# Kernel tuning notes

Hardware: AMD Instinct MI355X
Metric: run time of the kernel (lower is better)

The kernel has to match this reference:

```python
import jax, jax.numpy as jnp
import numpy as np

N, E = 100000, 1600000
IN_DIM, OUT_DIM, EDGE_DIM = 128, 64, 32
H, HD = 4, 16  # num_heads, head_dim; H*HD == OUT_DIM
NEG_SLOPE = 0.2


def setup_inputs() -> dict:
    key = jax.random.key(0)
    ks = jax.random.split(key, 9)
    return {
        "node_feat": jax.random.normal(ks[0], (N, IN_DIM), jnp.float32),
        "edge_feat": jax.random.normal(ks[1], (E, EDGE_DIM), jnp.float32),
        "W_src": jax.random.normal(ks[2], (OUT_DIM, IN_DIM), jnp.float32) * (2.0 / np.sqrt(IN_DIM + OUT_DIM)),
        "W_dst": jax.random.normal(ks[3], (OUT_DIM, IN_DIM), jnp.float32) * (2.0 / np.sqrt(IN_DIM + OUT_DIM)),
        "W_edge": jax.random.normal(ks[4], (OUT_DIM, EDGE_DIM), jnp.float32) * (2.0 / np.sqrt(EDGE_DIM + OUT_DIM)),
        "attn": jax.random.normal(ks[5], (1, H, HD), jnp.float32) * (2.0 / np.sqrt(1 + HD)),
        "bias": jnp.zeros((OUT_DIM,), jnp.float32),
        "src": jax.random.randint(ks[6], (E,), 0, N, jnp.int32),
        "dst": jax.random.randint(ks[7], (E,), 0, N, jnp.int32),
    }


def reference(node_feat, edge_feat, W_src, W_dst, W_edge, attn, bias, src, dst):
    n = node_feat.shape[0]
    # Linear projections (dropout is identity in eval mode / p=0)
    feat_src = (node_feat @ W_src.T).reshape(n, H, HD)  # [N,H,HD]
    feat_dst = (node_feat @ W_dst.T).reshape(n, H, HD)  # [N,H,HD]
    e_edge = (edge_feat @ W_edge.T).reshape(-1, H, HD)  # [E,H,HD]

    # u_add_v gather + edge feature injection, GATv2 nonlinearity then attn dot
    e = feat_src[src] + feat_dst[dst] + e_edge          # [E,H,HD]
    e = jax.nn.leaky_relu(e, NEG_SLOPE)
    logits = jnp.sum(e * attn, axis=-1)                 # [E,H]

    # edge softmax: normalize over edges sharing the same destination node
    seg_max = jax.ops.segment_max(logits, dst, num_segments=n)      # [N,H]
    ex = jnp.exp(logits - seg_max[dst])                             # [E,H]
    seg_sum = jax.ops.segment_sum(ex, dst, num_segments=n)          # [N,H]
    alpha = ex / seg_sum[dst]                                       # [E,H]

    # u_mul_e message + sum-aggregate to destinations
    msg = feat_src[src] * alpha[:, :, None]                         # [E,H,HD]
    ft = jax.ops.segment_sum(msg.reshape(-1, H * HD), dst, num_segments=n)  # [N,OUT]
    rst = ft + bias
    return rst, alpha
```

## Files before the change

kernel.cpp:

```cpp
#include <hip/hip_runtime.h>
#include <hip/hip_bf16.h>

#define N_NODES 100000
#define N_EDGES 1600000
#define IN_DIM 128
#define OUT_DIM 64
#define EDGE_DIM 32
#define NH 4
#define HD 16
#define NEG_SLOPE 0.2f

#define W_SRC_ELEMS (OUT_DIM * IN_DIM)
#define W_EDGE_ELEMS (OUT_DIM * EDGE_DIM)
#define W_TOTAL (2 * W_SRC_ELEMS + W_EDGE_ELEMS)

typedef __attribute__((ext_vector_type(8))) short short8;
typedef __attribute__((ext_vector_type(4))) float floatx4;

__device__ __forceinline__ void cvt_hilo(const float* __restrict__ p, short8& hi, short8& lo)
{
    floatx4 x0 = *(const floatx4*)p;
    floatx4 x1 = *(const floatx4*)(p + 4);
    float v[8] = {x0[0], x0[1], x0[2], x0[3], x1[0], x1[1], x1[2], x1[3]};
#pragma unroll
    for (int j = 0; j < 8; ++j) {
        union { __hip_bfloat16 b; short s; } h, l;
        h.b = __float2bfloat16(v[j]);
        l.b = __float2bfloat16(v[j] - __bfloat162float(h.b));
        hi[j] = h.s;
        lo[j] = l.s;
    }
}

__device__ __forceinline__ void cvt_hilo_nt(const float* __restrict__ p, short8& hi, short8& lo)
{
    floatx4 x0 = __builtin_nontemporal_load((const floatx4*)p);
    floatx4 x1 = __builtin_nontemporal_load((const floatx4*)(p + 4));
    float v[8] = {x0[0], x0[1], x0[2], x0[3], x1[0], x1[1], x1[2], x1[3]};
#pragma unroll
    for (int j = 0; j < 8; ++j) {
        union { __hip_bfloat16 b; short s; } h, l;
        h.b = __float2bfloat16(v[j]);
        l.b = __float2bfloat16(v[j] - __bfloat162float(h.b));
        hi[j] = h.s;
        lo[j] = l.s;
    }
}

__global__ __launch_bounds__(256) void wsplit_kernel(
    const float* __restrict__ W_src,
    const float* __restrict__ W_dst,
    const float* __restrict__ W_edge,
    short* __restrict__ w_hi,
    short* __restrict__ w_lo)
{
    int g = blockIdx.x * 256 + threadIdx.x;
    if (g >= W_TOTAL) return;
    float v;
    if (g < W_SRC_ELEMS)            v = W_src[g];
    else if (g < 2 * W_SRC_ELEMS)   v = W_dst[g - W_SRC_ELEMS];
    else                            v = W_edge[g - 2 * W_SRC_ELEMS];
    union { __hip_bfloat16 b; short s; } h, l;
    h.b = __float2bfloat16(v);
    l.b = __float2bfloat16(v - __bfloat162float(h.b));
    w_hi[g] = h.s;
    w_lo[g] = l.s;
}

__global__ __launch_bounds__(64) void node_proj_kernel(
    const float* __restrict__ node_feat,
    const short* __restrict__ w_hi,
    const short* __restrict__ w_lo,
    float* __restrict__ feat_src,
    float* __restrict__ feat_dst)
{
    const int lane = threadIdx.x;
    const int col  = lane & 15;
    const int quad = lane >> 4;
    const int m0   = blockIdx.x * 16;

    floatx4 acc[8];
#pragma unroll
    for (int t = 0; t < 8; ++t) acc[t] = (floatx4){0.f, 0.f, 0.f, 0.f};

#pragma unroll
    for (int kc = 0; kc < 4; ++kc) {
        short8 ahi, alo;
        cvt_hilo_nt(node_feat + (size_t)(m0 + col) * IN_DIM + kc * 32 + quad * 8, ahi, alo);
#pragma unroll
        for (int t = 0; t < 8; ++t) {
            int o = (t < 4 ? 0 : OUT_DIM) + (t & 3) * 16 + col;
            size_t off = (size_t)o * IN_DIM + kc * 32 + quad * 8;
            short8 bhi = *(const short8*)(w_hi + off);
            short8 blo = *(const short8*)(w_lo + off);
            acc[t] = __builtin_amdgcn_mfma_f32_16x16x32_bf16(ahi, bhi, acc[t], 0, 0, 0);
            acc[t] = __builtin_amdgcn_mfma_f32_16x16x32_bf16(ahi, blo, acc[t], 0, 0, 0);
            acc[t] = __builtin_amdgcn_mfma_f32_16x16x32_bf16(alo, bhi, acc[t], 0, 0, 0);
        }
    }

#pragma unroll
    for (int t = 0; t < 8; ++t) {
        float* out = (t < 4) ? feat_src : feat_dst;
        int ob = (t & 3) * 16;
#pragma unroll
        for (int r = 0; r < 4; ++r) {
            int node = m0 + quad * 4 + r;
            out[(size_t)node * OUT_DIM + ob + col] = acc[t][r];
        }
    }
}

__global__ __launch_bounds__(256) void edge_logits_kernel(
    const float* __restrict__ edge_feat,
    const short* __restrict__ we_hi,
    const short* __restrict__ we_lo,
    const float* __restrict__ attn,
    const int* __restrict__ src,
    const int* __restrict__ dst,
    const float* __restrict__ feat_src,
    const float* __restrict__ feat_dst,
    float* __restrict__ ex_out,
    int* __restrict__ deg)
{
    const int lane = threadIdx.x & 63;
    const int wave = threadIdx.x >> 6;
    const int col  = lane & 15;
    const int quad = lane >> 4;
    const size_t ebase0 = ((size_t)blockIdx.x * 4 + wave) * 32;

    int s[2][4], d[2][4];
#pragma unroll
    for (int u = 0; u < 2; ++u)
#pragma unroll
        for (int r = 0; r < 4; ++r) {
            s[u][r] = __builtin_nontemporal_load(&src[ebase0 + u * 16 + quad * 4 + r]);
            d[u][r] = __builtin_nontemporal_load(&dst[ebase0 + u * 16 + quad * 4 + r]);
        }

    short8 ahi[2], alo[2];
#pragma unroll
    for (int u = 0; u < 2; ++u)
        cvt_hilo_nt(edge_feat + (ebase0 + u * 16 + col) * EDGE_DIM + quad * 8, ahi[u], alo[u]);

    float att[4];
#pragma unroll
    for (int t = 0; t < 4; ++t) att[t] = attn[t * 16 + col];

    floatx4 acc[2][4];
#pragma unroll
    for (int t = 0; t < 4; ++t) {
        size_t off = (size_t)(t * 16 + col) * EDGE_DIM + quad * 8;
        short8 bhi = *(const short8*)(we_hi + off);
        short8 blo = *(const short8*)(we_lo + off);
#pragma unroll
        for (int u = 0; u < 2; ++u) {
            floatx4 c = (floatx4){0.f, 0.f, 0.f, 0.f};
            c = __builtin_amdgcn_mfma_f32_16x16x32_bf16(ahi[u], bhi, c, 0, 0, 0);
            c = __builtin_amdgcn_mfma_f32_16x16x32_bf16(ahi[u], blo, c, 0, 0, 0);
            c = __builtin_amdgcn_mfma_f32_16x16x32_bf16(alo[u], bhi, c, 0, 0, 0);
            acc[u][t] = c;
        }
    }

    const int j = col;
    const int rsel = j >> 2;

#pragma unroll
    for (int u = 0; u < 2; ++u) {
        float p[16];
#pragma unroll
        for (int r = 0; r < 4; ++r)
#pragma unroll
            for (int t = 0; t < 4; ++t) {
                float v = acc[u][t][r]
                        + feat_src[(size_t)s[u][r] * OUT_DIM + t * 16 + col]
                        + feat_dst[(size_t)d[u][r] * OUT_DIM + t * 16 + col];
                v = (v > 0.f) ? v : NEG_SLOPE * v;
                p[r * 4 + t] = v * att[t];
            }

        {
            const bool u8 = (col & 8) != 0;
#pragma unroll
            for (int i = 0; i < 8; ++i) {
                float keep = u8 ? p[i + 8] : p[i];
                float send = u8 ? p[i] : p[i + 8];
                p[i] = keep + __shfl_xor(send, 8);
            }
            const bool u4 = (col & 4) != 0;
#pragma unroll
            for (int i = 0; i < 4; ++i) {
                float keep = u4 ? p[i + 4] : p[i];
                float send = u4 ? p[i] : p[i + 4];
                p[i] = keep + __shfl_xor(send, 4);
            }
            const bool u2 = (col & 2) != 0;
#pragma unroll
            for (int i = 0; i < 2; ++i) {
                float keep = u2 ? p[i + 2] : p[i];
                float send = u2 ? p[i] : p[i + 2];
                p[i] = keep + __shfl_xor(send, 2);
            }
            const bool u1 = (col & 1) != 0;
            {
                float keep = u1 ? p[1] : p[0];
                float send = u1 ? p[0] : p[1];
                p[0] = keep + __shfl_xor(send, 1);
            }
        }

        float ev = __expf(p[0]);
        __builtin_nontemporal_store(ev, &ex_out[(ebase0 + u * 16) * NH + lane]);

        int dd = d[u][0];
#pragma unroll
        for (int r = 1; r < 4; ++r) dd = (rsel == r) ? d[u][r] : dd;
        if ((j & 3) == 0) atomicAdd(&deg[dd], 1);
    }
}

#define SCAN_BLOCKS 98

__global__ __launch_bounds__(256) void scan_phase1(
    const int* __restrict__ deg, int* __restrict__ partial)
{
    __shared__ int red[256];
    const int tid = threadIdx.x;
    const int base = blockIdx.x * 1024 + tid * 4;
    int s = 0;
#pragma unroll
    for (int i = 0; i < 4; ++i) {
        int idx = base + i;
        if (idx < N_NODES) s += deg[idx];
    }
    red[tid] = s;
    __syncthreads();
    for (int off = 128; off > 0; off >>= 1) {
        if (tid < off) red[tid] += red[tid + off];
        __syncthreads();
    }
    if (tid == 0) partial[blockIdx.x] = red[0];
}

__global__ __launch_bounds__(128) void scan_phase2(
    const int* __restrict__ partial, int* __restrict__ block_off, int* __restrict__ row_ptr)
{
    __shared__ int buf[128];
    const int tid = threadIdx.x;
    buf[tid] = (tid < SCAN_BLOCKS) ? partial[tid] : 0;
    __syncthreads();
    for (int off = 1; off < 128; off <<= 1) {
        int v = buf[tid];
        int add = (tid >= off) ? buf[tid - off] : 0;
        __syncthreads();
        buf[tid] = v + add;
        __syncthreads();
    }
    if (tid < SCAN_BLOCKS) block_off[tid] = (tid > 0) ? buf[tid - 1] : 0;
    if (tid == 0) row_ptr[N_NODES] = N_EDGES;
}

__global__ __launch_bounds__(256) void scan_phase3(
    const int* __restrict__ deg, const int* __restrict__ block_off,
    int* __restrict__ row_ptr, int* __restrict__ cursor)
{
    __shared__ int tsum[256];
    const int tid = threadIdx.x;
    const int base = blockIdx.x * 1024 + tid * 4;
    int d[4];
    int s = 0;
#pragma unroll
    for (int i = 0; i < 4; ++i) {
        int idx = base + i;
        d[i] = (idx < N_NODES) ? deg[idx] : 0;
        s += d[i];
    }
    tsum[tid] = s;
    __syncthreads();
    for (int off = 1; off < 256; off <<= 1) {
        int v = tsum[tid];
        int add = (tid >= off) ? tsum[tid - off] : 0;
        __syncthreads();
        tsum[tid] = v + add;
        __syncthreads();
    }
    int prefix = block_off[blockIdx.x] + ((tid > 0) ? tsum[tid - 1] : 0);
#pragma unroll
    for (int i = 0; i < 4; ++i) {
        int idx = base + i;
        if (idx < N_NODES) {
            row_ptr[idx] = prefix;
            cursor[idx]  = prefix;
            prefix += d[i];
        }
    }
}

__global__ __launch_bounds__(256) void bucket_fill_kernel(
    const int* __restrict__ dst,
    const int* __restrict__ src,
    const float* __restrict__ ex,
    int* __restrict__ cursor,
    int* __restrict__ esrc,
    float* __restrict__ exb)
{
    int e = blockIdx.x * 256 + threadIdx.x;
    int pos = atomicAdd(&cursor[__builtin_nontemporal_load(&dst[e])], 1);
    __builtin_nontemporal_store(__builtin_nontemporal_load(&src[e]), &esrc[pos]);
    floatx4 v = __builtin_nontemporal_load((const floatx4*)ex + e);
    __builtin_nontemporal_store(v, (floatx4*)exb + pos);
}

__global__ __launch_bounds__(256) void aggregate_kernel(
    const int* __restrict__ row_ptr,
    const int* __restrict__ esrc,
    const float* __restrict__ exb,
    const float* __restrict__ feat_src,
    const float* __restrict__ bias,
    float* __restrict__ seg_sum,
    float* __restrict__ out)
{
    const int node = blockIdx.x * 4 + (threadIdx.x >> 6);
    if (node >= N_NODES) return;
    const int lane = threadIdx.x & 63;
    const int h = lane >> 4;

    const int start = row_ptr[node];
    const int end   = row_ptr[node + 1];

    float acc = 0.f;
    float ssum = 0.f;

    int j = start;
    for (; j + 8 <= end; j += 8) {
        int   s_[8];
        float e_[8];
        float f_[8];
#pragma unroll
        for (int i = 0; i < 8; ++i) s_[i] = __builtin_nontemporal_load(&esrc[j + i]);
#pragma unroll
        for (int i = 0; i < 8; ++i) e_[i] = __builtin_nontemporal_load(&exb[(size_t)(j + i) * NH + h]);
#pragma unroll
        for (int i = 0; i < 8; ++i) f_[i] = feat_src[(size_t)s_[i] * OUT_DIM + lane];
#pragma unroll
        for (int i = 0; i < 8; ++i) {
            acc = fmaf(f_[i], e_[i], acc);
            ssum += e_[i];
        }
    }
    for (; j + 4 <= end; j += 4) {
        int   s_[4];
        float e_[4];
        float f_[4];
#pragma unroll
        for (int i = 0; i < 4; ++i) s_[i] = __builtin_nontemporal_load(&esrc[j + i]);
#pragma unroll
        for (int i = 0; i < 4; ++i) e_[i] = __builtin_nontemporal_load(&exb[(size_t)(j + i) * NH + h]);
#pragma unroll
        for (int i = 0; i < 4; ++i) f_[i] = feat_src[(size_t)s_[i] * OUT_DIM + lane];
#pragma unroll
        for (int i = 0; i < 4; ++i) {
            acc = fmaf(f_[i], e_[i], acc);
            ssum += e_[i];
        }
    }
    for (; j < end; ++j) {
        int s = __builtin_nontemporal_load(&esrc[j]);
        float ev = __builtin_nontemporal_load(&exb[(size_t)j * NH + h]);
        acc = fmaf(feat_src[(size_t)s * OUT_DIM + lane], ev, acc);
        ssum += ev;
    }

    if ((lane & 15) == 0) seg_sum[(size_t)node * NH + h] = ssum;
    float inv = (ssum > 0.f) ? 1.f / ssum : 0.f;
    __builtin_nontemporal_store(fmaf(acc, inv, bias[lane]), &out[(size_t)node * OUT_DIM + lane]);
}

__global__ __launch_bounds__(256) void normalize_kernel(
    const float* __restrict__ seg_sum,
    const int* __restrict__ dst,
    float* __restrict__ alpha)
{
    int e = blockIdx.x * 256 + threadIdx.x;
    int d = __builtin_nontemporal_load(&dst[e]);
    floatx4 ex4 = __builtin_nontemporal_load((const floatx4*)alpha + e);
    floatx4 ss  = *((const floatx4*)seg_sum + d);
    floatx4 r;
    r[0] = ex4[0] / ss[0];
    r[1] = ex4[1] / ss[1];
    r[2] = ex4[2] / ss[2];
    r[3] = ex4[3] / ss[3];
    __builtin_nontemporal_store(r, (floatx4*)alpha + e);
}

extern "C" void kernel_launch(void* const* d_in, const int* in_sizes, int n_in,
                              void* d_out, int out_size, void* d_ws, size_t ws_size,
                              hipStream_t stream)
{
    const float* node_feat = (const float*)d_in[0];
    const float* edge_feat = (const float*)d_in[1];
    const float* W_src     = (const float*)d_in[2];
    const float* W_dst     = (const float*)d_in[3];
    const float* W_edge    = (const float*)d_in[4];
    const float* attn      = (const float*)d_in[5];
    const float* bias      = (const float*)d_in[6];
    const int* src = (const int*)d_in[7];
    const int* dst = (const int*)d_in[8];

    float* ws       = (float*)d_ws;
    float* feat_src = ws;
    float* feat_dst = feat_src + (size_t)N_NODES * OUT_DIM;
    float* exb      = feat_dst;
    float* seg_sum  = feat_dst + (size_t)N_NODES * OUT_DIM;
    int*   deg      = (int*)(seg_sum + (size_t)N_NODES * NH);
    int*   row_ptr  = deg + N_NODES;
    int*   cursor   = row_ptr + N_NODES + 1;
    int*   esrc     = cursor + N_NODES;
    int*   partial  = esrc + N_EDGES;
    int*   boff     = partial + 128;
    short* w_hi     = (short*)(boff + 128);
    short* w_lo     = w_hi + W_TOTAL;

    float* rst_out   = (float*)d_out;
    float* alpha_out = rst_out + (size_t)N_NODES * OUT_DIM;

    hipMemsetAsync(deg, 0, (size_t)N_NODES * sizeof(int), stream);

    wsplit_kernel<<<(W_TOTAL + 255) / 256, 256, 0, stream>>>(W_src, W_dst, W_edge, w_hi, w_lo);
    node_proj_kernel<<<N_NODES / 16, 64, 0, stream>>>(node_feat, w_hi, w_lo, feat_src, feat_dst);
    edge_logits_kernel<<<N_EDGES / 128, 256, 0, stream>>>(edge_feat,
                                                          w_hi + 2 * W_SRC_ELEMS, w_lo + 2 * W_SRC_ELEMS,
                                                          attn, src, dst,
                                                          feat_src, feat_dst, alpha_out, deg);
    scan_phase1<<<SCAN_BLOCKS, 256, 0, stream>>>(deg, partial);
    scan_phase2<<<1, 128, 0, stream>>>(partial, boff, row_ptr);
    scan_phase3<<<SCAN_BLOCKS, 256, 0, stream>>>(deg, boff, row_ptr, cursor);
    bucket_fill_kernel<<<N_EDGES / 256, 256, 0, stream>>>(dst, src, alpha_out, cursor, esrc, exb);
    aggregate_kernel<<<(N_NODES + 3) / 4, 256, 0, stream>>>(row_ptr, esrc, exb,
                                                            feat_src, bias, seg_sum, rst_out);
    normalize_kernel<<<N_EDGES / 256, 256, 0, stream>>>(seg_sum, dst, alpha_out);
}
```

Measured before the change: 736.7 us.

## Build CSR permutation first and compute edge logits in destination-sorted order

The destination histogram, scan and a permutation fill now run before the edge-logit kernel. That kernel then processes edges in CSR order, gathering edge_feat, src and dst through the permutation and writing exp-logits and source ids directly in sorted order. This removes the separate bucket-fill and normalize passes. Aggregation scatters normalized alpha back to original edge order in a workspace, which is then copied to the output. The cost is gathered edge_feat reads, an extra pass over dst for the histogram, scattered alpha writes, and a full device-to-device copy of alpha.

```diff
diff --git a/kernel.cpp b/kernel.cpp
--- a/kernel.cpp
+++ b/kernel.cpp
@@ -67,6 +67,21 @@
     w_lo[g] = l.s;
 }
 
+__global__ __launch_bounds__(256) void deg_hist_kernel(
+    const int* __restrict__ dst, int* __restrict__ deg)
+{
+    int e = blockIdx.x * 256 + threadIdx.x;
+    atomicAdd(&deg[dst[e]], 1);
+}
+
+__global__ __launch_bounds__(256) void perm_fill_kernel(
+    const int* __restrict__ dst, int* __restrict__ cursor, int* __restrict__ eidx)
+{
+    int e = blockIdx.x * 256 + threadIdx.x;
+    int pos = atomicAdd(&cursor[dst[e]], 1);
+    eidx[pos] = e;
+}
+
 __global__ __launch_bounds__(64) void node_proj_kernel(
     const float* __restrict__ node_feat,
     const short* __restrict__ w_hi,
@@ -120,28 +135,38 @@
     const int* __restrict__ dst,
     const float* __restrict__ feat_src,
     const float* __restrict__ feat_dst,
-    float* __restrict__ ex_out,
-    int* __restrict__ deg)
+    const int* __restrict__ eidx,
+    float* __restrict__ exb,
+    int* __restrict__ esrc)
 {
     const int lane = threadIdx.x & 63;
     const int wave = threadIdx.x >> 6;
     const int col  = lane & 15;
     const int quad = lane >> 4;
-    const size_t ebase0 = ((size_t)blockIdx.x * 4 + wave) * 32;
+    const size_t pbase0 = ((size_t)blockIdx.x * 4 + wave) * 32;
+
+    int e_col[2], e_q[2][4];
+#pragma unroll
+    for (int u = 0; u < 2; ++u) {
+        e_col[u] = eidx[pbase0 + u * 16 + col];
+#pragma unroll
+        for (int r = 0; r < 4; ++r)
+            e_q[u][r] = eidx[pbase0 + u * 16 + quad * 4 + r];
+    }
 
     int s[2][4], d[2][4];
 #pragma unroll
     for (int u = 0; u < 2; ++u)
 #pragma unroll
         for (int r = 0; r < 4; ++r) {
-            s[u][r] = __builtin_nontemporal_load(&src[ebase0 + u * 16 + quad * 4 + r]);
-            d[u][r] = __builtin_nontemporal_load(&dst[ebase0 + u * 16 + quad * 4 + r]);
+            s[u][r] = src[e_q[u][r]];
+            d[u][r] = dst[e_q[u][r]];
         }
 
     short8 ahi[2], alo[2];
 #pragma unroll
     for (int u = 0; u < 2; ++u)
-        cvt_hilo_nt(edge_feat + (ebase0 + u * 16 + col) * EDGE_DIM + quad * 8, ahi[u], alo[u]);
+        cvt_hilo_nt(edge_feat + (size_t)e_col[u] * EDGE_DIM + quad * 8, ahi[u], alo[u]);
 
     float att[4];
 #pragma unroll
@@ -211,12 +236,12 @@
         }
 
         float ev = __expf(p[0]);
-        __builtin_nontemporal_store(ev, &ex_out[(ebase0 + u * 16) * NH + lane]);
-
-        int dd = d[u][0];
-#pragma unroll
-        for (int r = 1; r < 4; ++r) dd = (rsel == r) ? d[u][r] : dd;
-        if ((j & 3) == 0) atomicAdd(&deg[dd], 1);
+        exb[(pbase0 + u * 16) * NH + lane] = ev;
+
+        int ss = s[u][0];
+#pragma unroll
+        for (int r = 1; r < 4; ++r) ss = (rsel == r) ? s[u][r] : ss;
+        if ((j & 3) == 0) esrc[pbase0 + u * 16 + quad * 4 + rsel] = ss;
     }
 }
 
@@ -297,34 +322,21 @@
     }
 }
 
-__global__ __launch_bounds__(256) void bucket_fill_kernel(
-    const int* __restrict__ dst,
-    const int* __restrict__ src,
-    const float* __restrict__ ex,
-    int* __restrict__ cursor,
-    int* __restrict__ esrc,
-    float* __restrict__ exb)
-{
-    int e = blockIdx.x * 256 + threadIdx.x;
-    int pos = atomicAdd(&cursor[__builtin_nontemporal_load(&dst[e])], 1);
-    __builtin_nontemporal_store(__builtin_nontemporal_load(&src[e]), &esrc[pos]);
-    floatx4 v = __builtin_nontemporal_load((const floatx4*)ex + e);
-    __builtin_nontemporal_store(v, (floatx4*)exb + pos);
-}
-
 __global__ __launch_bounds__(256) void aggregate_kernel(
     const int* __restrict__ row_ptr,
     const int* __restrict__ esrc,
     const float* __restrict__ exb,
+    const int* __restrict__ eidx,
     const float* __restrict__ feat_src,
     const float* __restrict__ bias,
-    float* __restrict__ seg_sum,
+    float* __restrict__ alpha_ws,
     float* __restrict__ out)
 {
     const int node = blockIdx.x * 4 + (threadIdx.x >> 6);
     if (node >= N_NODES) return;
     const int lane = threadIdx.x & 63;
-    const int h = lane >> 4;
+    const int h  = lane >> 4;
+    const int hd = lane & 15;
 
     const int start = row_ptr[node];
     const int end   = row_ptr[node + 1];
@@ -338,9 +350,9 @@
         float e_[8];
         float f_[8];
 #pragma unroll
-        for (int i = 0; i < 8; ++i) s_[i] = __builtin_nontemporal_load(&esrc[j + i]);
-#pragma unroll
-        for (int i = 0; i < 8; ++i) e_[i] = __builtin_nontemporal_load(&exb[(size_t)(j + i) * NH + h]);
+        for (int i = 0; i < 8; ++i) s_[i] = esrc[j + i];
+#pragma unroll
+        for (int i = 0; i < 8; ++i) e_[i] = exb[(size_t)(j + i) * NH + h];
 #pragma unroll
         for (int i = 0; i < 8; ++i) f_[i] = feat_src[(size_t)s_[i] * OUT_DIM + lane];
 #pragma unroll
@@ -354,9 +366,9 @@
         float e_[4];
         float f_[4];
 #pragma unroll
-        for (int i = 0; i < 4; ++i) s_[i] = __builtin_nontemporal_load(&esrc[j + i]);
-#pragma unroll
-        for (int i = 0; i < 4; ++i) e_[i] = __builtin_nontemporal_load(&exb[(size_t)(j + i) * NH + h]);
+        for (int i = 0; i < 4; ++i) s_[i] = esrc[j + i];
+#pragma unroll
+        for (int i = 0; i < 4; ++i) e_[i] = exb[(size_t)(j + i) * NH + h];
 #pragma unroll
         for (int i = 0; i < 4; ++i) f_[i] = feat_src[(size_t)s_[i] * OUT_DIM + lane];
 #pragma unroll
@@ -366,32 +378,19 @@
         }
     }
     for (; j < end; ++j) {
-        int s = __builtin_nontemporal_load(&esrc[j]);
-        float ev = __builtin_nontemporal_load(&exb[(size_t)j * NH + h]);
+        int s = esrc[j];
+        float ev = exb[(size_t)j * NH + h];
         acc = fmaf(feat_src[(size_t)s * OUT_DIM + lane], ev, acc);
         ssum += ev;
     }
 
-    if ((lane & 15) == 0) seg_sum[(size_t)node * NH + h] = ssum;
     float inv = (ssum > 0.f) ? 1.f / ssum : 0.f;
-    __builtin_nontemporal_store(fmaf(acc, inv, bias[lane]), &out[(size_t)node * OUT_DIM + lane]);
-}
-
-__global__ __launch_bounds__(256) void normalize_kernel(
-    const float* __restrict__ seg_sum,
-    const int* __restrict__ dst,
-    float* __restrict__ alpha)
-{
-    int e = blockIdx.x * 256 + threadIdx.x;
-    int d = __builtin_nontemporal_load(&dst[e]);
-    floatx4 ex4 = __builtin_nontemporal_load((const floatx4*)alpha + e);
-    floatx4 ss  = *((const floatx4*)seg_sum + d);
-    floatx4 r;
-    r[0] = ex4[0] / ss[0];
-    r[1] = ex4[1] / ss[1];
-    r[2] = ex4[2] / ss[2];
-    r[3] = ex4[3] / ss[3];
-    __builtin_nontemporal_store(r, (floatx4*)alpha + e);
+    out[(size_t)node * OUT_DIM + lane] = fmaf(acc, inv, bias[lane]);
+
+    for (int p = start + hd; p < end; p += 16) {
+        int e = eidx[p];
+        alpha_ws[(size_t)e * NH + h] = exb[(size_t)p * NH + h] * inv;
+    }
 }
 
 extern "C" void kernel_launch(void* const* d_in, const int* in_sizes, int n_in,
@@ -411,12 +410,12 @@
     float* ws       = (float*)d_ws;
     float* feat_src = ws;
     float* feat_dst = feat_src + (size_t)N_NODES * OUT_DIM;
-    float* exb      = feat_dst;
-    float* seg_sum  = feat_dst + (size_t)N_NODES * OUT_DIM;
-    int*   deg      = (int*)(seg_sum + (size_t)N_NODES * NH);
+    float* alpha_ws = feat_dst;
+    int*   deg      = (int*)(feat_dst + (size_t)N_NODES * OUT_DIM);
     int*   row_ptr  = deg + N_NODES;
     int*   cursor   = row_ptr + N_NODES + 1;
-    int*   esrc     = cursor + N_NODES;
+    int*   eidx     = cursor + N_NODES;
+    int*   esrc     = eidx + N_EDGES;
     int*   partial  = esrc + N_EDGES;
     int*   boff     = partial + 128;
     short* w_hi     = (short*)(boff + 128);
@@ -425,19 +424,23 @@
     float* rst_out   = (float*)d_out;
     float* alpha_out = rst_out + (size_t)N_NODES * OUT_DIM;
 
+    float* exb = alpha_out;
+
     hipMemsetAsync(deg, 0, (size_t)N_NODES * sizeof(int), stream);
 
     wsplit_kernel<<<(W_TOTAL + 255) / 256, 256, 0, stream>>>(W_src, W_dst, W_edge, w_hi, w_lo);
+    deg_hist_kernel<<<N_EDGES / 256, 256, 0, stream>>>(dst, deg);
+    scan_phase1<<<SCAN_BLOCKS, 256, 0, stream>>>(deg, partial);
+    scan_phase2<<<1, 128, 0, stream>>>(partial, boff, row_ptr);
+    scan_phase3<<<SCAN_BLOCKS, 256, 0, stream>>>(deg, boff, row_ptr, cursor);
+    perm_fill_kernel<<<N_EDGES / 256, 256, 0, stream>>>(dst, cursor, eidx);
     node_proj_kernel<<<N_NODES / 16, 64, 0, stream>>>(node_feat, w_hi, w_lo, feat_src, feat_dst);
     edge_logits_kernel<<<N_EDGES / 128, 256, 0, stream>>>(edge_feat,
                                                           w_hi + 2 * W_SRC_ELEMS, w_lo + 2 * W_SRC_ELEMS,
                                                           attn, src, dst,
-                                                          feat_src, feat_dst, alpha_out, deg);
-    scan_phase1<<<SCAN_BLOCKS, 256, 0, stream>>>(deg, partial);
-    scan_phase2<<<1, 128, 0, stream>>>(partial, boff, row_ptr);
-    scan_phase3<<<SCAN_BLOCKS, 256, 0, stream>>>(deg, boff, row_ptr, cursor);
-    bucket_fill_kernel<<<N_EDGES / 256, 256, 0, stream>>>(dst, src, alpha_out, cursor, esrc, exb);
-    aggregate_kernel<<<(N_NODES + 3) / 4, 256, 0, stream>>>(row_ptr, esrc, exb,
-                                                            feat_src, bias, seg_sum, rst_out);
-    normalize_kernel<<<N_EDGES / 256, 256, 0, stream>>>(seg_sum, dst, alpha_out);
-}
+                                                          feat_src, feat_dst, eidx, exb, esrc);
+    aggregate_kernel<<<(N_NODES + 3) / 4, 256, 0, stream>>>(row_ptr, esrc, exb, eidx,
+                                                            feat_src, bias, alpha_ws, rst_out);
+    hipMemcpyAsync(alpha_out, alpha_ws, (size_t)N_EDGES * NH * sizeof(float),
+                   hipMemcpyDeviceToDevice, stream);
+}
```

After: 769.0 us. +4.4%, slower.
